# Performance work log

Measured on AMD Instinct MI355X. Metric: run time of the kernel, lower is better.

The kernel has to match this reference:

```python
import jax, jax.numpy as jnp
import numpy as np
from jax import lax

B = 128      # graphs per batch
N = 68       # facial landmarks (num_nodes per graph)
C = 3        # input channels
P = 32       # PATCH_SIZE
K = 16       # NUM_KERNELS
FD = 64      # feature_dim
GH = 128     # gcn_hidden_dim
OUT = 2      # output_dim
EG = 8 * N   # edges per graph
T = B * N    # total nodes


def setup_inputs() -> dict:
    key = jax.random.key(0)
    ks = jax.random.split(key, 8)
    x = jax.random.normal(ks[0], (T, C, P, P), jnp.float32)
    e = jax.random.randint(ks[1], (2, B, EG), 0, N)
    offs = (jnp.arange(B) * N)[None, :, None]
    edge_index = (e + offs).reshape(2, -1)            # within-graph edges, global ids
    batch = jnp.repeat(jnp.arange(B), N)              # node -> graph id
    conv_w = jax.random.normal(ks[2], (N, K, C, 3, 3), jnp.float32) * 0.05
    conv_b = jnp.zeros((N, K), jnp.float32)
    lin1_w = jax.random.normal(ks[3], (N, K * (P // 2) * (P // 2), FD), jnp.float32) * 0.02
    lin1_b = jnp.zeros((N, FD), jnp.float32)
    gcn_w = jax.random.normal(ks[4], (FD, GH), jnp.float32) * 0.1
    gcn_b = jnp.zeros((GH,), jnp.float32)
    mlp_w1 = jax.random.normal(ks[5], (GH, GH // 2), jnp.float32) * 0.1
    mlp_b1 = jnp.zeros((GH // 2,), jnp.float32)
    mlp_w2 = jax.random.normal(ks[6], (GH // 2, OUT), jnp.float32) * 0.1
    mlp_b2 = jnp.zeros((OUT,), jnp.float32)
    return dict(x=x, edge_index=edge_index, batch=batch, conv_w=conv_w, conv_b=conv_b,
                lin1_w=lin1_w, lin1_b=lin1_b, gcn_w=gcn_w, gcn_b=gcn_b,
                mlp_w1=mlp_w1, mlp_b1=mlp_b1, mlp_w2=mlp_w2, mlp_b2=mlp_b2)


def reference(x, edge_index, batch, conv_w, conv_b, lin1_w, lin1_b,
              gcn_w, gcn_b, mlp_w1, mlp_b1, mlp_w2, mlp_b2):
    # --- per-node-type CNN routing (nodes are laid out [graph, local_index]) ---
    xr = x.reshape(B, N, C, P, P)

    def cnn_one(xn, w, b):           # xn: [B,C,P,P]  w: [K,C,3,3]
        y = lax.conv_general_dilated(xn, w, (1, 1), 'SAME',
                                     dimension_numbers=('NCHW', 'OIHW', 'NCHW'))
        return jax.nn.relu(y + b[None, :, None, None])

    a = jax.vmap(cnn_one, in_axes=(1, 0, 0), out_axes=1)(xr, conv_w, conv_b)  # [B,N,K,P,P]
    pooled = lax.reduce_window(a, -jnp.inf, lax.max,
                               (1, 1, 1, 2, 2), (1, 1, 1, 2, 2), 'VALID')     # [B,N,K,P/2,P/2]
    flat = pooled.reshape(B, N, -1)
    feats = jax.nn.relu(jnp.einsum('bnf,nfo->bno', flat, lin1_w) + lin1_b[None])  # [B,N,FD]
    nodes = feats.reshape(T, FD)

    # --- GCNConv: add self-loops, symmetric normalization ---
    loop = jnp.arange(T)
    src = jnp.concatenate([edge_index[0], loop])
    dst = jnp.concatenate([edge_index[1], loop])
    deg = jax.ops.segment_sum(jnp.ones_like(dst, jnp.float32), dst, T)
    dis = jnp.where(deg > 0, 1.0 / jnp.sqrt(deg), 0.0)
    norm = dis[src] * dis[dst]
    xw = nodes @ gcn_w                                   # [T,GH]
    h = jax.ops.segment_sum(norm[:, None] * xw[src], dst, T) + gcn_b
    h = jax.nn.relu(h)

    # --- global mean pool over graphs ---
    cnt = jax.ops.segment_sum(jnp.ones((T,), jnp.float32), batch, B)
    g = jax.ops.segment_sum(h, batch, B) / cnt[:, None]  # [B,GH]

    # --- MLP head ---
    z = jax.nn.relu(g @ mlp_w1 + mlp_b1)
    return z @ mlp_w2 + mlp_b2                           # [B,OUT]
```

## Files before the change

kernel.cpp:

```cpp
#include <hip/hip_runtime.h>
#include <hip/hip_fp16.h>

#define B_   128
#define N_   68
#define C_   3
#define P_   32
#define K_   16
#define FD_  64
#define GH_  128
#define EG_  544
#define T_   8704
#define FLAT_ 4096
#define FCH_ 16

typedef __attribute__((ext_vector_type(8))) _Float16 half8;
typedef __attribute__((ext_vector_type(2))) _Float16 half2v;
typedef __attribute__((ext_vector_type(4))) float   floatx4;

__global__ __launch_bounds__(256) void conv_pool_kernel(
    const float* __restrict__ x, const float* __restrict__ conv_w,
    const float* __restrict__ conv_b, _Float16* __restrict__ pooled) {
  const int t = blockIdx.x;
  const int n = t % N_;
  const int tid = threadIdx.x;

  __shared__ float xs[3 * 34 * 34];
  __shared__ float wS[K_ * 28];

  {
    const float* wp = conv_w + (size_t)n * (K_ * 27);
    const float* bp = conv_b + (size_t)n * K_;
    for (int i = tid; i < K_ * 28; i += 256) {
      int k = i / 28, j = i - k * 28;
      wS[i] = (j < 27) ? wp[k * 27 + j] : bp[k];
    }
  }
  for (int i = tid; i < 396; i += 256) {
    int c = i / 132, j = i - c * 132;
    int off;
    if (j < 34)       off = j;
    else if (j < 68)  off = 33 * 34 + (j - 34);
    else if (j < 100) off = (j - 68 + 1) * 34;
    else              off = (j - 100 + 1) * 34 + 33;
    xs[c * 1156 + off] = 0.0f;
  }
  const float4* xg = (const float4*)(x + (size_t)t * (C_ * P_ * P_));
  #pragma unroll
  for (int j = 0; j < 3; j++) {
    int i4 = tid + j * 256;
    float4 v = xg[i4];
    int f0 = i4 * 4;
    int c = f0 >> 10, rem = f0 & 1023, y = rem >> 5, xc = rem & 31;
    float* dstp = &xs[c * 1156 + (y + 1) * 34 + xc + 1];
    dstp[0] = v.x; dstp[1] = v.y; dstp[2] = v.z; dstp[3] = v.w;
  }
  __syncthreads();

  const int py = tid >> 4, px = tid & 15;

  float xr[3][4][4];
  #pragma unroll
  for (int c = 0; c < 3; c++)
    #pragma unroll
    for (int r = 0; r < 4; r++)
      #pragma unroll
      for (int cc = 0; cc < 4; cc++)
        xr[c][r][cc] = xs[c * 1156 + (2 * py + r) * 34 + (2 * px + cc)];

  _Float16* outp = pooled + (size_t)t * FLAT_ + py * 16 + px;

  #pragma unroll 2
  for (int k = 0; k < K_; k++) {
    float w[28];
    const float4* wk4 = (const float4*)&wS[k * 28];
    #pragma unroll
    for (int q4 = 0; q4 < 7; q4++) *(float4*)&w[q4 * 4] = wk4[q4];
    float bk = w[27];
    float a00 = bk, a01 = bk, a10 = bk, a11 = bk;
    #pragma unroll
    for (int c = 0; c < 3; c++)
      #pragma unroll
      for (int dy = 0; dy < 3; dy++)
        #pragma unroll
        for (int dx = 0; dx < 3; dx++) {
          float wv = w[c * 9 + dy * 3 + dx];
          a00 += xr[c][dy][dx]         * wv;
          a01 += xr[c][dy][dx + 1]     * wv;
          a10 += xr[c][dy + 1][dx]     * wv;
          a11 += xr[c][dy + 1][dx + 1] * wv;
        }
    float m = fmaxf(fmaxf(a00, a01), fmaxf(a10, a11));
    m = fmaxf(m, 0.0f);
    outp[k * 256] = (_Float16)m;
  }
}

__global__ __launch_bounds__(256) void lin1_mfma_kernel(
    const _Float16* __restrict__ pooled, const float* __restrict__ lin1_w,
    float* __restrict__ part) {
  const int n   = blockIdx.x >> 4;
  const int fc  = blockIdx.x & 15;
  const int tid = threadIdx.x;
  const int wave = tid >> 6, lane = tid & 63;
  const int q = lane >> 4, lr = lane & 15;

  __shared__ __align__(16) _Float16 As[128 * 72];
  __shared__ __align__(16) _Float16 Bt[64 * 72];

  floatx4 acc[2][4];
  #pragma unroll
  for (int mt = 0; mt < 2; mt++)
    #pragma unroll
    for (int nt = 0; nt < 4; nt++)
      acc[mt][nt] = (floatx4){0.f, 0.f, 0.f, 0.f};

  const int f_base = fc * 256;
  for (int step = 0; step < 4; step++) {
    const int f0 = f_base + step * 64;

    #pragma unroll
    for (int j = 0; j < 4; j++) {
      int idx = tid + j * 256;
      int r = idx >> 3, ch = idx & 7;
      uint4 v = *(const uint4*)&pooled[(size_t)(r * N_ + n) * FLAT_ + f0 + ch * 8];
      *(uint4*)&As[r * 72 + ch * 8] = v;
    }
    const float* wg = &lin1_w[(size_t)n * (FLAT_ * FD_) + (size_t)f0 * FD_];
    #pragma unroll
    for (int it = 0; it < 2; it++) {
      int p = tid + it * 256;
      int o0 = (p & 15) * 4, k0 = (p >> 4) * 2;
      const float* wgk = wg + k0 * 64 + o0;
      float4 va = *(const float4*)wgk;
      float4 vb = *(const float4*)(wgk + 64);
      *(half2v*)&Bt[(o0 + 0) * 72 + k0] = (half2v){(_Float16)va.x, (_Float16)vb.x};
      *(half2v*)&Bt[(o0 + 1) * 72 + k0] = (half2v){(_Float16)va.y, (_Float16)vb.y};
      *(half2v*)&Bt[(o0 + 2) * 72 + k0] = (half2v){(_Float16)va.z, (_Float16)vb.z};
      *(half2v*)&Bt[(o0 + 3) * 72 + k0] = (half2v){(_Float16)va.w, (_Float16)vb.w};
    }
    __syncthreads();

    #pragma unroll
    for (int kh = 0; kh < 2; kh++) {
      half8 af[2], bf[4];
      #pragma unroll
      for (int mt = 0; mt < 2; mt++)
        af[mt] = *(const half8*)&As[(wave * 32 + mt * 16 + lr) * 72 + kh * 32 + q * 8];
      #pragma unroll
      for (int nt = 0; nt < 4; nt++)
        bf[nt] = *(const half8*)&Bt[(nt * 16 + lr) * 72 + kh * 32 + q * 8];
      #pragma unroll
      for (int mt = 0; mt < 2; mt++)
        #pragma unroll
        for (int nt = 0; nt < 4; nt++)
          acc[mt][nt] = __builtin_amdgcn_mfma_f32_16x16x32_f16(
              af[mt], bf[nt], acc[mt][nt], 0, 0, 0);
    }
    __syncthreads();
  }

  float* pb = part + (size_t)fc * T_ * FD_;
  #pragma unroll
  for (int mt = 0; mt < 2; mt++) {
    #pragma unroll
    for (int v = 0; v < 4; v++) {
      int r = wave * 32 + mt * 16 + q * 4 + v;
      size_t base = (size_t)(r * N_ + n) * FD_;
      #pragma unroll
      for (int nt = 0; nt < 4; nt++)
        pb[base + nt * 16 + lr] = acc[mt][nt][v];
    }
  }
}

__global__ __launch_bounds__(256) void feats_kernel(
    const float* __restrict__ part, const float* __restrict__ lin1_b,
    float* __restrict__ feats) {
  int gid = blockIdx.x * 256 + threadIdx.x;
  int t = gid >> 4, f4 = (gid & 15) * 4;
  int n = t % N_;
  float4 s = *(const float4*)&lin1_b[n * FD_ + f4];
  #pragma unroll
  for (int fc = 0; fc < FCH_; fc++) {
    float4 v = *(const float4*)&part[((size_t)fc * T_ + t) * FD_ + f4];
    s.x += v.x; s.y += v.y; s.z += v.z; s.w += v.w;
  }
  s.x = fmaxf(s.x, 0.f); s.y = fmaxf(s.y, 0.f);
  s.z = fmaxf(s.z, 0.f); s.w = fmaxf(s.w, 0.f);
  *(float4*)&feats[(size_t)t * FD_ + f4] = s;
}

__global__ __launch_bounds__(256) void gcn_agg_kernel(
    const float* __restrict__ feats, const int* __restrict__ edge_index,
    float* __restrict__ agg) {
  const int b  = blockIdx.x >> 1;
  const int fh = blockIdx.x & 1;
  const int tid = threadIdx.x;

  __shared__ float fS[N_ * 33], aS[N_ * 33];
  __shared__ int   esrcS[EG_], edstS[EG_];
  __shared__ float nrmS[EG_];
  __shared__ int   degS[N_];
  __shared__ float disS[N_];

  if (tid < N_) degS[tid] = 0;
  const int* srcp = edge_index;
  const int* dstp = edge_index + (B_ * EG_);
  const int e0 = b * EG_, nbase = b * N_;
  for (int e = tid; e < EG_; e += 256) {
    esrcS[e] = srcp[e0 + e] - nbase;
    edstS[e] = dstp[e0 + e] - nbase;
  }
  for (int idx = tid; idx < N_ * 32; idx += 256) {
    int i = idx >> 5, f = idx & 31;
    fS[i * 33 + f] = feats[(size_t)(b * N_ + i) * FD_ + fh * 32 + f];
  }
  __syncthreads();
  for (int e = tid; e < EG_; e += 256) atomicAdd(&degS[edstS[e]], 1);
  __syncthreads();
  if (tid < N_) disS[tid] = rsqrtf((float)(degS[tid] + 1));
  __syncthreads();
  for (int e = tid; e < EG_; e += 256)
    nrmS[e] = disS[esrcS[e]] * disS[edstS[e]];
  for (int idx = tid; idx < N_ * 32; idx += 256) {
    int i = idx >> 5, f = idx & 31;
    float d = disS[i];
    aS[i * 33 + f] = d * d * fS[i * 33 + f];
  }
  __syncthreads();
  for (int idx = tid; idx < EG_ * 32; idx += 256) {
    int e = idx >> 5, f = idx & 31;
    atomicAdd(&aS[edstS[e] * 33 + f], nrmS[e] * fS[esrcS[e] * 33 + f]);
  }
  __syncthreads();
  for (int idx = tid; idx < N_ * 32; idx += 256) {
    int i = idx >> 5, f = idx & 31;
    agg[(size_t)(b * N_ + i) * FD_ + fh * 32 + f] = aS[i * 33 + f];
  }
}

__global__ __launch_bounds__(512) void gcn_head_kernel(
    const float* __restrict__ agg, const float* __restrict__ gcn_w,
    const float* __restrict__ gcn_b, const float* __restrict__ w1,
    const float* __restrict__ b1, const float* __restrict__ w2,
    const float* __restrict__ b2, float* __restrict__ out) {
  const int b = blockIdx.x;
  const int tid = threadIdx.x;

  __shared__ float aS[N_ * 68];
  __shared__ float wS[FD_ * GH_];
  __shared__ float gP[4][GH_];
  __shared__ float z1S[64];

  for (int i4 = tid; i4 < N_ * 16; i4 += 512) {
    int i = i4 >> 4, qf = (i4 & 15) * 4;
    *(float4*)&aS[i * 68 + qf] = *(const float4*)&agg[(size_t)(b * N_ + i) * FD_ + qf];
  }
  #pragma unroll
  for (int j = 0; j < 4; j++)
    ((float4*)wS)[tid + j * 512] = ((const float4*)gcn_w)[tid + j * 512];
  __syncthreads();

  const int j = tid & 127, ig = tid >> 7;
  float wc[64];
  #pragma unroll
  for (int k = 0; k < 64; k++) wc[k] = wS[k * GH_ + j];
  const float bias = gcn_b[j];
  float gsum = 0.f;
  for (int i = ig; i < N_; i += 4) {
    float acc = bias;
    #pragma unroll
    for (int kq = 0; kq < 16; kq++) {
      float4 a = *(const float4*)&aS[i * 68 + kq * 4];
      acc += a.x * wc[kq * 4] + a.y * wc[kq * 4 + 1]
           + a.z * wc[kq * 4 + 2] + a.w * wc[kq * 4 + 3];
    }
    gsum += fmaxf(acc, 0.f);
  }
  gP[ig][j] = gsum;
  __syncthreads();
  if (tid < GH_)
    gP[0][tid] = (gP[0][tid] + gP[1][tid] + gP[2][tid] + gP[3][tid]) * (1.f / 68.f);
  __syncthreads();
  if (tid < 64) {
    float s = b1[tid];
    #pragma unroll 8
    for (int jj = 0; jj < GH_; jj++) s += gP[0][jj] * w1[jj * 64 + tid];
    z1S[tid] = fmaxf(s, 0.f);
  }
  __syncthreads();
  if (tid < 2) {
    float s = b2[tid];
    #pragma unroll 8
    for (int jj = 0; jj < 64; jj++) s += z1S[jj] * w2[jj * 2 + tid];
    out[b * 2 + tid] = s;
  }
}

extern "C" void kernel_launch(void* const* d_in, const int* in_sizes, int n_in,
                              void* d_out, int out_size, void* d_ws, size_t ws_size,
                              hipStream_t stream) {
  const float* x        = (const float*)d_in[0];
  const int*   edge_idx = (const int*)d_in[1];
  const float* conv_w   = (const float*)d_in[3];
  const float* conv_b   = (const float*)d_in[4];
  const float* lin1_w   = (const float*)d_in[5];
  const float* lin1_b   = (const float*)d_in[6];
  const float* gcn_w    = (const float*)d_in[7];
  const float* gcn_b    = (const float*)d_in[8];
  const float* mlp_w1   = (const float*)d_in[9];
  const float* mlp_b1   = (const float*)d_in[10];
  const float* mlp_w2   = (const float*)d_in[11];
  const float* mlp_b2   = (const float*)d_in[12];
  float* outp = (float*)d_out;

  char* wsb = (char*)d_ws;
  _Float16* pooled = (_Float16*)wsb;
  float* part  = (float*)(wsb + (size_t)T_ * FLAT_ * 2);
  float* feats = part + (size_t)FCH_ * T_ * FD_;
  float* agg   = feats + (size_t)T_ * FD_;

  conv_pool_kernel<<<T_, 256, 0, stream>>>(x, conv_w, conv_b, pooled);
  lin1_mfma_kernel<<<N_ * FCH_, 256, 0, stream>>>(pooled, lin1_w, part);
  feats_kernel<<<544, 256, 0, stream>>>(part, lin1_b, feats);
  gcn_agg_kernel<<<B_ * 2, 256, 0, stream>>>(feats, edge_idx, agg);
  gcn_head_kernel<<<B_, 512, 0, stream>>>(agg, gcn_w, gcn_b,
                                          mlp_w1, mlp_b1, mlp_w2, mlp_b2, outp);
}
```

Measured before the change: 355.6 us.

## Recast conv+pool as fp16 MFMA with shifted weight matrices

Rewrites the per-node 3x3 conv plus 2x2 max-pool as MFMA 16x16x32 fp16 matrix ops instead of scalar FMAs. Weights are packed into shifted A-matrices, one per horizontal sub-pixel offset, with a separate correction matrix for the 27th tap. The input tile is staged in LDS as fp16 instead of fp32. This targets the scalar FMA cost of the conv kernel at the price of fp16 rounding on inputs and weights, plus extra setup for packing the weights into LDS.

```diff
diff --git a/kernel.cpp b/kernel.cpp
--- a/kernel.cpp
+++ b/kernel.cpp
@@ -16,6 +16,9 @@
 typedef __attribute__((ext_vector_type(8))) _Float16 half8;
 typedef __attribute__((ext_vector_type(2))) _Float16 half2v;
 typedef __attribute__((ext_vector_type(4))) float   floatx4;
+typedef __attribute__((ext_vector_type(4))) unsigned int uint32x4;
+
+#define XPITCH 1164
 
 __global__ __launch_bounds__(256) void conv_pool_kernel(
     const float* __restrict__ x, const float* __restrict__ conv_w,
@@ -24,17 +27,32 @@
   const int n = t % N_;
   const int tid = threadIdx.x;
 
-  __shared__ float xs[3 * 34 * 34];
-  __shared__ float wS[K_ * 28];
-
-  {
-    const float* wp = conv_w + (size_t)n * (K_ * 27);
-    const float* bp = conv_b + (size_t)n * K_;
-    for (int i = tid; i < K_ * 28; i += 256) {
-      int k = i / 28, j = i - k * 28;
-      wS[i] = (j < 27) ? wp[k * 27 + j] : bp[k];
-    }
-  }
+  __shared__ _Float16 xsh[3 * XPITCH];
+  __shared__ __align__(16) _Float16 wAS[2][16][32];
+  __shared__ __align__(16) _Float16 wCS[2][16][32];
+  __shared__ __align__(16) float bS[16];
+
+  const float* wp = conv_w + (size_t)n * (K_ * 27);
+
+  for (int i = tid; i < 1024; i += 256) {
+    int sx = i >> 9, k = (i >> 5) & 15, slot = i & 31;
+    int q = slot >> 3, r = (slot >> 2) & 1, col = slot & 3;
+    int cr = q * 2 + r, c = cr / 3, dy = cr - c * 3, dx = col - sx;
+    float v = (dx >= 0 && dx < 3) ? wp[k * 27 + c * 9 + dy * 3 + dx] : 0.0f;
+    wAS[sx][k][slot] = (_Float16)v;
+  }
+  for (int i = tid; i < 1024; i += 256) {
+    int sx = i >> 9, k = (i >> 5) & 15, slot = i & 31;
+    int q = slot >> 3, j = slot & 7;
+    float v = 0.0f;
+    if (q == 0 && j < 4) {
+      int dx = j - sx;
+      if (dx >= 0 && dx < 3) v = wp[k * 27 + 2 * 9 + 2 * 3 + dx];
+    }
+    wCS[sx][k][slot] = (_Float16)v;
+  }
+  if (tid < 16) bS[tid] = conv_b[(size_t)n * K_ + tid];
+
   for (int i = tid; i < 396; i += 256) {
     int c = i / 132, j = i - c * 132;
     int off;
@@ -42,7 +60,7 @@
     else if (j < 68)  off = 33 * 34 + (j - 34);
     else if (j < 100) off = (j - 68 + 1) * 34;
     else              off = (j - 100 + 1) * 34 + 33;
-    xs[c * 1156 + off] = 0.0f;
+    xsh[c * XPITCH + off] = (_Float16)0.0f;
   }
   const float4* xg = (const float4*)(x + (size_t)t * (C_ * P_ * P_));
   #pragma unroll
@@ -51,47 +69,68 @@
     float4 v = xg[i4];
     int f0 = i4 * 4;
     int c = f0 >> 10, rem = f0 & 1023, y = rem >> 5, xc = rem & 31;
-    float* dstp = &xs[c * 1156 + (y + 1) * 34 + xc + 1];
-    dstp[0] = v.x; dstp[1] = v.y; dstp[2] = v.z; dstp[3] = v.w;
-  }
-  __syncthreads();
-
-  const int py = tid >> 4, px = tid & 15;
-
-  float xr[3][4][4];
-  #pragma unroll
-  for (int c = 0; c < 3; c++)
-    #pragma unroll
-    for (int r = 0; r < 4; r++)
-      #pragma unroll
-      for (int cc = 0; cc < 4; cc++)
-        xr[c][r][cc] = xs[c * 1156 + (2 * py + r) * 34 + (2 * px + cc)];
-
-  _Float16* outp = pooled + (size_t)t * FLAT_ + py * 16 + px;
-
-  #pragma unroll 2
-  for (int k = 0; k < K_; k++) {
-    float w[28];
-    const float4* wk4 = (const float4*)&wS[k * 28];
-    #pragma unroll
-    for (int q4 = 0; q4 < 7; q4++) *(float4*)&w[q4 * 4] = wk4[q4];
-    float bk = w[27];
-    float a00 = bk, a01 = bk, a10 = bk, a11 = bk;
-    #pragma unroll
-    for (int c = 0; c < 3; c++)
-      #pragma unroll
-      for (int dy = 0; dy < 3; dy++)
-        #pragma unroll
-        for (int dx = 0; dx < 3; dx++) {
-          float wv = w[c * 9 + dy * 3 + dx];
-          a00 += xr[c][dy][dx]         * wv;
-          a01 += xr[c][dy][dx + 1]     * wv;
-          a10 += xr[c][dy + 1][dx]     * wv;
-          a11 += xr[c][dy + 1][dx + 1] * wv;
-        }
-    float m = fmaxf(fmaxf(a00, a01), fmaxf(a10, a11));
-    m = fmaxf(m, 0.0f);
-    outp[k * 256] = (_Float16)m;
+    _Float16* dp = &xsh[c * XPITCH + (y + 1) * 34 + xc + 1];
+    dp[0] = (_Float16)v.x; dp[1] = (_Float16)v.y;
+    dp[2] = (_Float16)v.z; dp[3] = (_Float16)v.w;
+  }
+  __syncthreads();
+
+  const int lane = tid & 63, wave = tid >> 6;
+  const int lr = lane & 15, q = lane >> 4;
+  const int ldy = lr >> 3, ldx = lr & 7;
+
+  half8 aMain0 = *(const half8*)&wAS[0][lr][q * 8];
+  half8 aMain1 = *(const half8*)&wAS[1][lr][q * 8];
+  half8 aCorr0 = *(const half8*)&wCS[0][lr][q * 8];
+  half8 aCorr1 = *(const half8*)&wCS[1][lr][q * 8];
+  floatx4 cbias = *(const floatx4*)&bS[q * 4];
+
+  const int crL = q * 2, crH = crL + 1;
+  const int cL = crL / 3, dyL = crL - cL * 3;
+  const int cH = crH / 3, dyH = crH - cH * 3;
+  const _Float16* chL = &xsh[cL * XPITCH + dyL * 34];
+  const _Float16* chH = &xsh[cH * XPITCH + dyH * 34];
+  const _Float16* chC = &xsh[2 * XPITCH + 2 * 34];
+
+  #pragma unroll
+  for (int i = 0; i < 4; i++) {
+    const int qq = wave * 4 + i;
+    const int py0 = (qq >> 1) * 2, px0 = (qq & 1) * 8;
+    const int py = py0 + ldy, px = px0 + ldx;
+    const int ebase = py * 68 + px * 2;
+    const _Float16* pL = chL + ebase;
+    const _Float16* pH = chH + ebase;
+    const _Float16* pC = chC + ebase;
+
+    floatx4 mx;
+    #pragma unroll
+    for (int sy = 0; sy < 2; sy++) {
+      unsigned int uL0 = *(const unsigned int*)&pL[sy * 34];
+      unsigned int uL1 = *(const unsigned int*)&pL[sy * 34 + 2];
+      unsigned int uH0 = *(const unsigned int*)&pH[sy * 34];
+      unsigned int uH1 = *(const unsigned int*)&pH[sy * 34 + 2];
+      unsigned int uC0 = *(const unsigned int*)&pC[sy * 34];
+      unsigned int uC1 = *(const unsigned int*)&pC[sy * 34 + 2];
+      half8 bMain = __builtin_bit_cast(half8, (uint32x4){uL0, uL1, uH0, uH1});
+      half8 bCorr = __builtin_bit_cast(half8, (uint32x4){uC0, uC1, uC0, uC1});
+      floatx4 d0 = __builtin_amdgcn_mfma_f32_16x16x32_f16(aCorr0, bCorr, cbias, 0, 0, 0);
+      d0 = __builtin_amdgcn_mfma_f32_16x16x32_f16(aMain0, bMain, d0, 0, 0, 0);
+      floatx4 d1 = __builtin_amdgcn_mfma_f32_16x16x32_f16(aCorr1, bCorr, cbias, 0, 0, 0);
+      d1 = __builtin_amdgcn_mfma_f32_16x16x32_f16(aMain1, bMain, d1, 0, 0, 0);
+      floatx4 m;
+      m[0] = fmaxf(d0[0], d1[0]); m[1] = fmaxf(d0[1], d1[1]);
+      m[2] = fmaxf(d0[2], d1[2]); m[3] = fmaxf(d0[3], d1[3]);
+      if (sy == 0) mx = m;
+      else {
+        mx[0] = fmaxf(mx[0], m[0]); mx[1] = fmaxf(mx[1], m[1]);
+        mx[2] = fmaxf(mx[2], m[2]); mx[3] = fmaxf(mx[3], m[3]);
+      }
+    }
+    _Float16* op = pooled + (size_t)t * FLAT_ + q * 1024 + py * 16 + px;
+    op[0]   = (_Float16)fmaxf(mx[0], 0.0f);
+    op[256] = (_Float16)fmaxf(mx[1], 0.0f);
+    op[512] = (_Float16)fmaxf(mx[2], 0.0f);
+    op[768] = (_Float16)fmaxf(mx[3], 0.0f);
   }
 }
 
```

Measured after the change: 315.3 us. 1.13x faster.
